# Performance work log

Hardware: AMD Instinct MI355X
Metric: run time of the kernel (lower is better)

Reference implementation:

```python
import jax, jax.numpy as jnp
import numpy as np
from jax import lax

CORR = 16  # corr_size in the original module


def _adaptive_pool16(x):
    # exact adaptive avg pool when H, W divisible by 16 (torch-equivalent)
    B, C, H, W = x.shape
    return x.reshape(B, C, CORR, H // CORR, CORR, W // CORR).mean(axis=(3, 5))


def _l2_normalize(x, eps=1e-12):
    # torch F.normalize default: L2 over dim=1, norm clamped to eps
    n = jnp.sqrt(jnp.sum(x * x, axis=1, keepdims=True))
    return x / jnp.maximum(n, eps)


def _instance_norm(x, eps=1e-5):
    # InstanceNorm2d, affine=False, biased variance over H,W per (b,c)
    mu = x.mean(axis=(2, 3), keepdims=True)
    var = jnp.mean((x - mu) ** 2, axis=(2, 3), keepdims=True)
    return (x - mu) * lax.rsqrt(var + eps)


def _corr_reduce(x, W1, b1, W2, b2):
    # 1x1 conv (256 -> fc) + bias
    y = jnp.einsum('bchw,oc->bohw', x, W1[:, :, 0, 0]) + b1[None, :, None, None]
    y = jax.nn.relu(_instance_norm(y))
    # 3x3 conv, padding=1, stride=1
    y = lax.conv_general_dilated(y, W2, (1, 1), 'SAME',
                                 dimension_numbers=('NCHW', 'OIHW', 'NCHW'))
    return y + b2[None, :, None, None]


def _corr(feat):
    # pooled [B,C,16,16] used as per-sample bank of 256 1x1 conv kernels
    pooled = _adaptive_pool16(feat)                      # [B,C,16,16]
    norm = _l2_normalize(feat)                           # [B,C,H,W]
    B, C = pooled.shape[:2]
    ker = pooled.reshape(B, C, CORR * CORR)              # [B,C,256]
    # corr[b,p,h,w] = sum_c ker[b,c,p] * norm[b,c,h,w]
    return jnp.einsum('bcp,bchw->bphw', ker, norm)


def setup_inputs() -> dict:
    key = jax.random.key(0)
    ks = jax.random.split(key, 6)
    B, C, H, W = 16, 256, 96, 96
    fc = 256
    return {
        'F_infrared': jax.random.normal(ks[0], (B, C, H, W), jnp.float32),
        'F_visible': jax.random.normal(ks[1], (B, C, H, W), jnp.float32),
        'W1': jax.random.normal(ks[2], (fc, CORR * CORR, 1, 1), jnp.float32) * 0.05,
        'b1': jax.random.normal(ks[3], (fc,), jnp.float32) * 0.05,
        'W2': jax.random.normal(ks[4], (fc, fc, 3, 3), jnp.float32) * 0.05,
        'b2': jax.random.normal(ks[5], (fc,), jnp.float32) * 0.05,
    }


def reference(F_infrared, F_visible, W1, b1, W2, b2):
    VIS_corr = _corr_reduce(_corr(F_visible), W1, b1, W2, b2)
    IR_corr = _corr_reduce(_corr(F_infrared), W1, b1, W2, b2)
    return (IR_corr, VIS_corr)
```

## Files before the change

### kernel.cpp

```cpp
#include <hip/hip_runtime.h>
#include <hip/hip_bf16.h>

#define BATCH 16
#define CH    256
#define HH    96
#define WW    96
#define HWSZ  9216
#define FCH   256
#define PP    256

typedef float f32x4 __attribute__((ext_vector_type(4)));
typedef short bf16x8 __attribute__((ext_vector_type(8)));
typedef unsigned short ushortT;

#define APAD_ELEMS 2458624
#define APAD_CHUNKS 307328

__device__ __forceinline__ void gload16(const void* g, void* l) {
    __builtin_amdgcn_global_load_lds((const __attribute__((address_space(1))) void*)g,
                                     (__attribute__((address_space(3))) void*)l, 16, 0, 0);
}
__device__ __forceinline__ float bfu2f(ushortT u) {
    return __uint_as_float(((unsigned)u) << 16);
}
__device__ __forceinline__ ushortT f2bfu(float f) {
    __hip_bfloat16 hb = __float2bfloat16(f);
    return *reinterpret_cast<ushortT*>(&hb);
}

__global__ void fpack_k(const float* __restrict__ feat, ushortT* __restrict__ fpack,
                        float* __restrict__ rnorm)
{
    int b = blockIdx.y;
    int hw = blockIdx.x * 256 + threadIdx.x;
    const float* src = feat + (size_t)b * CH * HWSZ + hw;
    uint4* dst = (uint4*)fpack + (size_t)b * 32 * HWSZ + hw;
    float ss = 0.f;
    for (int cb = 0; cb < 32; ++cb) {
        union { ushortT u[8]; uint4 v; } pk;
#pragma unroll
        for (int i = 0; i < 8; ++i) {
            float v = src[(size_t)(cb * 8 + i) * HWSZ];
            ss += v * v;
            pk.u[i] = f2bfu(v);
        }
        dst[(size_t)cb * HWSZ] = pk.v;
    }
    rnorm[b * HWSZ + hw] = 1.0f / fmaxf(sqrtf(ss), 1e-12f);
}

__global__ void pool16b_k(const ushortT* __restrict__ fpack, float* __restrict__ pooled)
{
    int cb = blockIdx.x, b = blockIdx.y;
    const uint4* fp = (const uint4*)fpack + ((size_t)b * 32 + cb) * HWSZ;
    int t = threadIdx.x;
    int pr = t >> 4, pc = t & 15;
    float s[8] = {};
#pragma unroll
    for (int i = 0; i < 6; ++i) {
#pragma unroll
        for (int j = 0; j < 6; ++j) {
            uint4 v = fp[(pr * 6 + i) * WW + pc * 6 + j];
            const ushortT* u = (const ushortT*)&v;
#pragma unroll
            for (int k = 0; k < 8; ++k) s[k] += bfu2f(u[k]);
        }
    }
#pragma unroll
    for (int k = 0; k < 8; ++k)
        pooled[((size_t)b * CH + cb * 8 + k) * PP + t] = s[k] * (1.0f / 36.0f);
}

__global__ void gemmM_k(const float* __restrict__ W1, const float* __restrict__ pooled,
                        ushortT* __restrict__ Mb16)
{
    int b = blockIdx.z;
    int o0 = blockIdx.y * 16, c0 = blockIdx.x * 16;
    int ty = threadIdx.y, tx = threadIdx.x;
    __shared__ float Ws[16][17], Ps[16][17];
    float acc = 0.f;
    for (int p0 = 0; p0 < PP; p0 += 16) {
        Ws[ty][tx] = W1[(o0 + ty) * PP + p0 + tx];
        Ps[ty][tx] = pooled[((size_t)b * CH + (c0 + ty)) * PP + p0 + tx];
        __syncthreads();
#pragma unroll
        for (int p = 0; p < 16; ++p) acc += Ws[ty][p] * Ps[tx][p];
        __syncthreads();
    }
    int c = c0 + tx, o = o0 + ty;
    Mb16[(((size_t)b * 32 + (c >> 3)) * 256 + o) * 8 + (c & 7)] = f2bfu(acc);
}

__global__ void repack_w2_k(const float* __restrict__ W2, ushortT* __restrict__ W2r2)
{
    int e = blockIdx.x * 256 + threadIdx.x;
    int ci = e & 7, o = (e >> 3) & 255, cb = (e >> 11) & 31, s = e >> 16;
    int c = cb * 8 + ci;
    W2r2[e] = f2bfu(W2[((size_t)o * 256 + c) * 9 + s]);
}

__global__ void zborder_k(uint4* __restrict__ apad)
{
    int bl = blockIdx.x;
    uint4* apC = apad + (size_t)bl * APAD_CHUNKS;
    uint4 z; z.x = 0; z.y = 0; z.z = 0; z.w = 0;
    for (int e = threadIdx.x; e < 3136; e += 256) {
        apC[e] = z;
        apC[(size_t)97 * 32 * 98 + e] = z;
    }
    for (int e = threadIdx.x; e < 3072; e += 256) {
        int row = 1 + (e >> 5), cb = e & 31;
        size_t base = (size_t)(row * 32 + cb) * 98;
        apC[base] = z;
        apC[base + 97] = z;
    }
}

__global__ __launch_bounds__(256, 4) void gemmYm_k(const ushortT* __restrict__ Mb16,
                                                   const ushortT* __restrict__ fpack,
                                                   const float* __restrict__ rnorm,
                                                   ushortT* __restrict__ apad,
                                                   float* __restrict__ ps,
                                                   float* __restrict__ ps2, int b0)
{
    int bl = blockIdx.z, bg = b0 + bl;
    int hw0 = blockIdx.x * 128;
    int o0 = blockIdx.y * 128;
    int tid = threadIdx.x, wave = tid >> 6, lane = tid & 63;
    int wm = wave >> 1, wn = wave & 1;
    int lr = lane & 15, kb = lane >> 4;

    __shared__ __align__(16) char smem[33280];

    const uint4* MbC = (const uint4*)Mb16 + (size_t)bg * 32 * 256;
    const uint4* fpC = (const uint4*)fpack + (size_t)bg * 32 * HWSZ;

    f32x4 acc[4][4] = {};

    auto STAGE = [&](int buf, int s) {
        int cb0 = s * 4;
        uint4* A = (uint4*)smem + (size_t)buf * 1024;
        uint4* B = A + 512;
#pragma unroll
        for (int i = 0; i < 2; ++i) {
            int e = tid + i * 256;
            int kk = e >> 7, j = e & 127;
            gload16(MbC + (size_t)(cb0 + kk) * 256 + o0 + j, A + e);
            gload16(fpC + (size_t)(cb0 + kk) * HWSZ + hw0 + j, B + e);
        }
    };

    STAGE(0, 0);
    for (int s = 0; s < 8; ++s) {
        int buf = s & 1;
        __syncthreads();
        if (s < 7) STAGE(buf ^ 1, s + 1);
        const bf16x8* AsV = (const bf16x8*)(smem + (size_t)buf * 16384);
        const bf16x8* BsV = AsV + 512;
        bf16x8 af[4], bfv[4];
#pragma unroll
        for (int mf = 0; mf < 4; ++mf) af[mf] = AsV[kb * 128 + wm * 64 + mf * 16 + lr];
#pragma unroll
        for (int nf = 0; nf < 4; ++nf) bfv[nf] = BsV[kb * 128 + wn * 64 + nf * 16 + lr];
#pragma unroll
        for (int mf = 0; mf < 4; ++mf)
#pragma unroll
            for (int nf = 0; nf < 4; ++nf)
                acc[mf][nf] = __builtin_amdgcn_mfma_f32_16x16x32_bf16(af[mf], bfv[nf], acc[mf][nf], 0, 0, 0);
    }
    __syncthreads();

    float rn[4];
#pragma unroll
    for (int nf = 0; nf < 4; ++nf)
        rn[nf] = rnorm[(size_t)bg * HWSZ + hw0 + wn * 64 + nf * 16 + lr];

    {
        float sA[4][4], sB[4][4];
#pragma unroll
        for (int mf = 0; mf < 4; ++mf)
#pragma unroll
            for (int r = 0; r < 4; ++r) {
                float s1 = 0.f, s2 = 0.f;
#pragma unroll
                for (int nf = 0; nf < 4; ++nf) {
                    float v = acc[mf][nf][r] * rn[nf];
                    s1 += v; s2 += v * v;
                }
#pragma unroll
                for (int off = 8; off > 0; off >>= 1) {
                    s1 += __shfl_down(s1, off, 16);
                    s2 += __shfl_down(s2, off, 16);
                }
                sA[mf][r] = s1; sB[mf][r] = s2;
            }
        if (lr == 0) {
            int col = blockIdx.x * 2 + wn;
#pragma unroll
            for (int mf = 0; mf < 4; ++mf)
#pragma unroll
                for (int r = 0; r < 4; ++r) {
                    int og = o0 + wm * 64 + mf * 16 + kb * 4 + r;
                    size_t idx = ((size_t)bl * 256 + og) * 144 + col;
                    ps[idx]  = sA[mf][r];
                    ps2[idx] = sB[mf][r];
                }
        }
    }

    ushortT* T = (ushortT*)smem;
#pragma unroll
    for (int mf = 0; mf < 4; ++mf)
#pragma unroll
        for (int nf = 0; nf < 4; ++nf)
#pragma unroll
            for (int r = 0; r < 4; ++r)
                T[(wn * 64 + nf * 16 + lr) * 130 + wm * 64 + mf * 16 + kb * 4 + r] =
                    f2bfu(acc[mf][nf][r] * rn[nf]);
    __syncthreads();

    uint4* apC = (uint4*)apad + (size_t)bl * APAD_CHUNKS;
    int ob0 = blockIdx.y * 16;
#pragma unroll
    for (int i = 0; i < 8; ++i) {
        int e = tid + i * 256;
        int hw_l = e >> 4, ob = e & 15;
        uint4 v = *(uint4*)&T[hw_l * 130 + ob * 8];
        int hw = hw0 + hw_l;
        int h = hw / 96, w = hw - h * 96;
        apC[(size_t)((h + 1) * 32 + ob0 + ob) * 98 + (w + 1)] = v;
    }
}

__global__ void finstats_k(const float* __restrict__ ps, const float* __restrict__ ps2,
                           float* __restrict__ mu, float* __restrict__ istd)
{
    int bl = blockIdx.x, o = threadIdx.x;
    const float* p1 = ps  + ((size_t)bl * 256 + o) * 144;
    const float* p2 = ps2 + ((size_t)bl * 256 + o) * 144;
    float S = 0.f, S2 = 0.f;
    for (int i = 0; i < 144; ++i) { S += p1[i]; S2 += p2[i]; }
    float m   = S * (1.0f / HWSZ);
    float var = S2 * (1.0f / HWSZ) - m * m;
    if (var < 0.f) var = 0.f;
    mu[bl * 256 + o]   = m;
    istd[bl * 256 + o] = rsqrtf(var + 1e-5f);
}

__global__ void nr_k(ushortT* __restrict__ apad, const float* __restrict__ mu,
                     const float* __restrict__ istd)
{
    int row = blockIdx.x + 1, bl = blockIdx.y;
    __shared__ float smu[256], sis[256];
    smu[threadIdx.x] = mu[bl * 256 + threadIdx.x];
    sis[threadIdx.x] = istd[bl * 256 + threadIdx.x];
    __syncthreads();
    uint4* apC = (uint4*)apad + (size_t)bl * APAD_CHUNKS + (size_t)row * 32 * 98;
    for (int e = threadIdx.x; e < 3072; e += 256) {
        int ob = e / 96;
        int w = e - ob * 96 + 1;
        uint4 v = apC[(size_t)ob * 98 + w];
        ushortT* u = (ushortT*)&v;
#pragma unroll
        for (int k = 0; k < 8; ++k) {
            float f = (bfu2f(u[k]) - smu[ob * 8 + k]) * sis[ob * 8 + k];
            u[k] = f2bfu(f > 0.f ? f : 0.f);
        }
        apC[(size_t)ob * 98 + w] = v;
    }
}

__global__ __launch_bounds__(256, 2) void conv3m7_k(const ushortT* __restrict__ apad,
                                                    const ushortT* __restrict__ W2r2,
                                                    const float* __restrict__ b2,
                                                    float* __restrict__ out, int swz)
{
    int ht, ot, bl;
    if (swz) {
        int lin = blockIdx.x + 24 * (blockIdx.y + 4 * blockIdx.z);
        int xcd = lin & 7, i = lin >> 3;
        int second = (i >= 96) ? 1 : 0;
        bl = 2 * xcd + second;
        int w = i - second * 96;
        ot = w / 24; ht = w - ot * 24;
    } else {
        ht = blockIdx.x; ot = blockIdx.y; bl = blockIdx.z;
    }
    int h0 = ht * 4;
    int o0 = ot * 64;
    int tid = threadIdx.x;
    int wave = tid >> 6, lane = tid & 63;
    int lr = lane & 15, kb = lane >> 4;

    __shared__ __align__(16) uint4 BsC[2560];

    const uint4* apadC = (const uint4*)apad + (size_t)bl * APAD_CHUNKS;
    const bf16x8* w2V  = (const bf16x8*)W2r2;
    const bf16x8* BsV  = (const bf16x8*)BsC;

    f32x4 acc[4][6] = {};

    for (int ci = 0; ci < 8; ++ci) {
        int cb0 = ci * 4;
        __syncthreads();
#pragma unroll
        for (int i = 0; i < 10; ++i) {
            int e = tid + i * 256;
            int se = e < 2352 ? e : e - 256;
            int w = se % 98, r = se / 98;
            int kk = r & 3, row = r >> 2;
            gload16(apadC + (size_t)((h0 + row) * 32 + cb0 + kk) * 98 + w,
                    &BsC[e]);
        }
        __syncthreads();
#pragma unroll 1
        for (int kh = 0; kh < 3; ++kh) {
            bf16x8 aR[3][4];
#pragma unroll
            for (int kw = 0; kw < 3; ++kw)
#pragma unroll
                for (int mf = 0; mf < 4; ++mf)
                    aR[kw][mf] = w2V[(size_t)((kh * 3 + kw) * 32 + cb0 + kb) * 256
                                     + o0 + mf * 16 + lr];
#pragma unroll
            for (int kw = 0; kw < 3; ++kw) {
#pragma unroll
                for (int nf = 0; nf < 6; ++nf) {
                    bf16x8 bfr = BsV[((wave + kh) * 4 + kb) * 98 + nf * 16 + lr + kw];
#pragma unroll
                    for (int mf = 0; mf < 4; ++mf)
                        acc[mf][nf] = __builtin_amdgcn_mfma_f32_16x16x32_bf16(aR[kw][mf], bfr, acc[mf][nf], 0, 0, 0);
                }
            }
        }
    }

    int h = h0 + wave;
    float* obase = out + (size_t)bl * FCH * HWSZ + (size_t)h * WW;
#pragma unroll
    for (int mf = 0; mf < 4; ++mf) {
#pragma unroll
        for (int r = 0; r < 4; ++r) {
            int o = o0 + mf * 16 + kb * 4 + r;
            float bias = b2[o];
            float* orow = obase + (size_t)o * HWSZ;
#pragma unroll
            for (int nf = 0; nf < 6; ++nf)
                orow[nf * 16 + lr] = acc[mf][nf][r] + bias;
        }
    }
}

extern "C" void kernel_launch(void* const* d_in, const int* in_sizes, int n_in,
                              void* d_out, int out_size, void* d_ws, size_t ws_size,
                              hipStream_t stream)
{
    const float* Fir  = (const float*)d_in[0];
    const float* Fvis = (const float*)d_in[1];
    const float* W1   = (const float*)d_in[2];
    const float* W2   = (const float*)d_in[4];
    const float* b2   = (const float*)d_in[5];
    float* out = (float*)d_out;

    char* w = (char*)d_ws;
    const size_t poolB = (size_t)BATCH * CH * PP * 4;
    const size_t MbB   = (size_t)BATCH * 32 * 256 * 8 * 2;
    const size_t rnB   = (size_t)BATCH * HWSZ * 4;
    const size_t stB   = (size_t)BATCH * FCH * 4;
    const size_t w2rB  = (size_t)9 * 32 * 256 * 8 * 2;
    const size_t psB   = (size_t)BATCH * 256 * 144 * 4;
    const size_t fpB   = (size_t)BATCH * 32 * HWSZ * 8 * 2;

    size_t off = 0;
    float*   pooled = (float*)(w + off);   off += poolB;
    ushortT* Mb16   = (ushortT*)(w + off); off += MbB;
    float*   rnorm  = (float*)(w + off);   off += rnB;
    float*   mu     = (float*)(w + off);   off += stB;
    float*   istd   = (float*)(w + off);   off += stB;
    ushortT* W2r2   = (ushortT*)(w + off); off += w2rB;
    float*   ps     = (float*)(w + off);   off += psB;
    float*   ps2    = (float*)(w + off);   off += psB;
    ushortT* fpack  = (ushortT*)(w + off); off += fpB;
    const size_t fixed = off;

    const size_t apadB = (size_t)APAD_ELEMS * 2;
    size_t avail = ws_size > fixed ? ws_size - fixed : 0;
    int NB = (int)(avail / apadB);
    if (NB > BATCH) NB = BATCH;
    if (NB < 1) NB = 1;
    ushortT* apad = (ushortT*)(w + fixed);

    repack_w2_k<<<2304, 256, 0, stream>>>(W2, W2r2);
    zborder_k<<<NB, 256, 0, stream>>>((uint4*)apad);

    for (int f = 0; f < 2; ++f) {
        const float* feat = (f == 0) ? Fir : Fvis;
        float* o_ = out + (size_t)f * BATCH * FCH * HWSZ;

        fpack_k<<<dim3(36, BATCH), 256, 0, stream>>>(feat, fpack, rnorm);
        pool16b_k<<<dim3(32, BATCH), 256, 0, stream>>>(fpack, pooled);
        gemmM_k<<<dim3(16, 16, BATCH), dim3(16, 16), 0, stream>>>(W1, pooled, Mb16);

        for (int b0 = 0; b0 < BATCH; b0 += NB) {
            int nb = BATCH - b0 < NB ? BATCH - b0 : NB;
            gemmYm_k<<<dim3(72, 2, nb), 256, 0, stream>>>(Mb16, fpack, rnorm, apad,
                                                          ps, ps2, b0);
            finstats_k<<<nb, 256, 0, stream>>>(ps, ps2, mu, istd);
            nr_k<<<dim3(96, nb), 256, 0, stream>>>(apad, mu, istd);
            conv3m7_k<<<dim3(24, 4, nb), 256, 0, stream>>>(apad, W2r2, b2,
                                                           o_ + (size_t)b0 * FCH * HWSZ,
                                                           nb == 16 ? 1 : 0);
        }
    }
}
```

Baseline: 719.8 us.

## Stage conv weights in LDS and drop XCD block swizzle in 3x3 conv

The 3x3 conv kernel now loads the weight slice for each channel chunk into shared memory with async global-to-LDS loads, instead of having every wave read weights straight from global memory into registers. The kh loop is fully unrolled and the XCD-aware block remapping is removed in favour of plain grid indexing. The store in the Y GEMM epilogue is also reordered so consecutive threads write consecutive w positions of a channel block. This trades more LDS use (about 74 KB per block) and possible occupancy loss for less redundant global weight traffic, and it may lose L2 locality now that the swizzle is gone.

Result: faster. 671.9 us (-6.7%).

```diff
diff --git a/kernel.cpp b/kernel.cpp
--- a/kernel.cpp
+++ b/kernel.cpp
@@ -224,7 +224,7 @@
 #pragma unroll
     for (int i = 0; i < 8; ++i) {
         int e = tid + i * 256;
-        int hw_l = e >> 4, ob = e & 15;
+        int ob = e >> 7, hw_l = e & 127;
         uint4 v = *(uint4*)&T[hw_l * 130 + ob * 8];
         int hw = hw0 + hw_l;
         int h = hw / 96, w = hw - h * 96;
@@ -270,33 +270,25 @@
     }
 }
 
-__global__ __launch_bounds__(256, 2) void conv3m7_k(const ushortT* __restrict__ apad,
+__global__ __launch_bounds__(256, 2) void conv3m4_k(const ushortT* __restrict__ apad,
                                                     const ushortT* __restrict__ W2r2,
                                                     const float* __restrict__ b2,
-                                                    float* __restrict__ out, int swz)
-{
-    int ht, ot, bl;
-    if (swz) {
-        int lin = blockIdx.x + 24 * (blockIdx.y + 4 * blockIdx.z);
-        int xcd = lin & 7, i = lin >> 3;
-        int second = (i >= 96) ? 1 : 0;
-        bl = 2 * xcd + second;
-        int w = i - second * 96;
-        ot = w / 24; ht = w - ot * 24;
-    } else {
-        ht = blockIdx.x; ot = blockIdx.y; bl = blockIdx.z;
-    }
-    int h0 = ht * 4;
-    int o0 = ot * 64;
+                                                    float* __restrict__ out)
+{
+    int h0 = blockIdx.x * 4;
+    int o0 = blockIdx.y * 64;
+    int bl = blockIdx.z;
     int tid = threadIdx.x;
     int wave = tid >> 6, lane = tid & 63;
     int lr = lane & 15, kb = lane >> 4;
 
-    __shared__ __align__(16) uint4 BsC[2560];
+    __shared__ __align__(16) uint4 AsC[2304];
+    __shared__ __align__(16) uint4 BsC[2368];
 
     const uint4* apadC = (const uint4*)apad + (size_t)bl * APAD_CHUNKS;
-    const bf16x8* w2V  = (const bf16x8*)W2r2;
-    const bf16x8* BsV  = (const bf16x8*)BsC;
+    const uint4* w2C   = (const uint4*)W2r2;
+    const bf16x8* AsV = (const bf16x8*)AsC;
+    const bf16x8* BsV = (const bf16x8*)BsC;
 
     f32x4 acc[4][6] = {};
 
@@ -304,32 +296,37 @@
         int cb0 = ci * 4;
         __syncthreads();
 #pragma unroll
+        for (int i = 0; i < 9; ++i) {
+            int e = tid + i * 256;
+            int o = e & 63, kk = (e >> 6) & 3, s = e >> 8;
+            gload16(w2C + (size_t)(s * 32 + cb0 + kk) * 256 + o0 + o, &AsC[e]);
+        }
+#pragma unroll
         for (int i = 0; i < 10; ++i) {
             int e = tid + i * 256;
-            int se = e < 2352 ? e : e - 256;
-            int w = se % 98, r = se / 98;
-            int kk = r & 3, row = r >> 2;
-            gload16(apadC + (size_t)((h0 + row) * 32 + cb0 + kk) * 98 + w,
-                    &BsC[e]);
+            if (e < 2352) {
+                int w = e % 98, r = e / 98;
+                int kk = r & 3, row = r >> 2;
+                gload16(apadC + (size_t)((h0 + row) * 32 + cb0 + kk) * 98 + w,
+                        &BsC[e]);
+            }
         }
         __syncthreads();
-#pragma unroll 1
+#pragma unroll
         for (int kh = 0; kh < 3; ++kh) {
-            bf16x8 aR[3][4];
-#pragma unroll
-            for (int kw = 0; kw < 3; ++kw)
+#pragma unroll
+            for (int kw = 0; kw < 3; ++kw) {
+                int s = kh * 3 + kw;
+                bf16x8 af[4];
 #pragma unroll
                 for (int mf = 0; mf < 4; ++mf)
-                    aR[kw][mf] = w2V[(size_t)((kh * 3 + kw) * 32 + cb0 + kb) * 256
-                                     + o0 + mf * 16 + lr];
-#pragma unroll
-            for (int kw = 0; kw < 3; ++kw) {
+                    af[mf] = AsV[(s * 4 + kb) * 64 + mf * 16 + lr];
 #pragma unroll
                 for (int nf = 0; nf < 6; ++nf) {
                     bf16x8 bfr = BsV[((wave + kh) * 4 + kb) * 98 + nf * 16 + lr + kw];
 #pragma unroll
                     for (int mf = 0; mf < 4; ++mf)
-                        acc[mf][nf] = __builtin_amdgcn_mfma_f32_16x16x32_bf16(aR[kw][mf], bfr, acc[mf][nf], 0, 0, 0);
+                        acc[mf][nf] = __builtin_amdgcn_mfma_f32_16x16x32_bf16(af[mf], bfr, acc[mf][nf], 0, 0, 0);
                 }
             }
         }
@@ -407,9 +404,8 @@
                                                           ps, ps2, b0);
             finstats_k<<<nb, 256, 0, stream>>>(ps, ps2, mu, istd);
             nr_k<<<dim3(96, nb), 256, 0, stream>>>(apad, mu, istd);
-            conv3m7_k<<<dim3(24, 4, nb), 256, 0, stream>>>(apad, W2r2, b2,
-                                                           o_ + (size_t)b0 * FCH * HWSZ,
-                                                           nb == 16 ? 1 : 0);
-        }
-    }
-}
+            conv3m4_k<<<dim3(24, 4, nb), 256, 0, stream>>>(apad, W2r2, b2,
+                                                           o_ + (size_t)b0 * FCH * HWSZ);
+        }
+    }
+}
```
